# Kernel optimization log

Hardware: AMD Instinct MI355X
Metric: run time of the kernel (lower is better)

The kernel has to match this reference:

```python
import jax, jax.numpy as jnp
import numpy as np
import math

D_MODEL = 512; NHEAD = 8; D_HEAD = 64; C_OUT = 64
SEQ_LEN = 1024; PRED_LEN = 256; K = 8; DIM_FF = 2048
LOW_FREQ = 1; EPS = 1e-5
BATCH = 8


def _next_fast_len(n):
    # smallest 5-smooth integer >= n (matches scipy.fftpack.next_fast_len)
    while True:
        m = n
        for p in (2, 3, 5):
            while m % p == 0:
                m //= p
        if m == 1:
            return n
        n += 1


def _conv1d_fft(f, g, n):
    # matches torch conv1d_fft with N == M == n along axis 1 (cross-correlation via conj)
    fast_len = _next_fast_len(2 * n - 1)
    Ff = jnp.fft.rfft(f, n=fast_len, axis=1)
    Fg = jnp.fft.rfft(g, n=fast_len, axis=1)
    out = jnp.fft.irfft(Ff * jnp.conj(Fg), n=fast_len, axis=1)
    out = jnp.roll(out, -1, axis=1)
    return out[:, fast_len - n:fast_len]


def _exp_smooth(values, sw, v0, aux_values=None):
    # values: (b,t,h,d); sw: (h,1); v0: (1,1,h,d or 1)
    b, t, h, d = values.shape
    alpha = jax.nn.sigmoid(sw)                        # (h,1)
    powers = jnp.arange(t, dtype=values.dtype)
    weight = (1.0 - alpha) * alpha ** powers[::-1]    # (h,t)
    init_w = alpha ** (powers + 1.0)                  # (h,t)
    weight = weight.T[None, :, :, None]               # (1,t,h,1)
    init_w = init_w.T[None, :, :, None]
    out = init_w * v0 + _conv1d_fft(values, weight, t)
    if aux_values is not None:
        aux_w = weight * (alpha / (1.0 - alpha))[None, None, :, :]
        out = out + _conv1d_fft(aux_values, aux_w, t)
    return out


def _layer_norm(x, g, b):
    mu = x.mean(-1, keepdims=True)
    var = ((x - mu) ** 2).mean(-1, keepdims=True)
    return (x - mu) * jax.lax.rsqrt(var + EPS) * g + b


def _fourier_season(x):
    b, t, d = x.shape
    xf = jnp.fft.rfft(x, axis=1)                      # (b, t//2+1, d) complex
    hi = xf.shape[1] - 1 if t % 2 == 0 else xf.shape[1]
    xf = xf[:, LOW_FREQ:hi]                           # (b, F, d)
    freqs = (jnp.arange(t // 2 + 1, dtype=x.dtype) / t)[LOW_FREQ:hi]
    # top-K frequencies per (batch, feature) by amplitude
    _, idx = jax.lax.top_k(jnp.abs(jnp.moveaxis(xf, 1, 2)), K)   # (b,d,K)
    idx = jnp.moveaxis(idx, 2, 1)                     # (b,K,d)
    x_sel = jnp.take_along_axis(xf, idx, axis=1)      # (b,K,d) complex
    f_sel = freqs[idx]                                # (b,K,d)
    # trig re-synthesis / extrapolation over t + PRED_LEN steps
    x_all = jnp.concatenate([x_sel, jnp.conj(x_sel)], axis=1)    # (b,2K,d)
    f_all = jnp.concatenate([f_sel, -f_sel], axis=1)[:, :, None, :]  # (b,2K,1,d)
    t_val = jnp.arange(t + PRED_LEN, dtype=x.dtype).reshape(1, 1, -1, 1)
    amp = (jnp.abs(x_all) / t)[:, :, None, :]
    phase = jnp.angle(x_all)[:, :, None, :]
    x_time = amp * jnp.cos(2.0 * math.pi * f_all * t_val + phase)  # (b,2K,T,d)
    return x_time.sum(axis=1)                         # (b, t+PRED_LEN, d)


def _growth_layer(x, z0, in_w, in_b, sw, v0, out_w, out_b):
    b, t, _ = x.shape
    v = (x @ in_w.T + in_b).reshape(b, t, NHEAD, D_HEAD)
    v = jnp.concatenate([jnp.broadcast_to(z0[None, None], (b, 1, NHEAD, D_HEAD)), v], axis=1)
    v = v[:, 1:] - v[:, :-1]                          # first differences, (b,t,h,dh)
    s = _exp_smooth(v, sw, v0)
    s = jnp.concatenate([jnp.broadcast_to(v0, (b, 1, NHEAD, D_HEAD)), s], axis=1)  # (b,t+1,h,dh)
    return s.reshape(b, t + 1, NHEAD * D_HEAD) @ out_w.T + out_b


def _level_layer(level, growth, season, sw, v0, gw, gb, spw, spb):
    b, t, _ = level.shape
    g = (growth @ gw.T + gb)[..., None]               # (b,t,c,1)
    s = (season @ spw.T + spb)[..., None]             # (b,t,c,1)
    l = level[..., None] - s
    out = _exp_smooth(l, sw, v0, aux_values=g)        # (b,t,c,1)
    return out[..., 0]


def _forward(res, level, gl_z0, gl_in_w, gl_in_b, gl_sw, gl_v0, gl_out_w, gl_out_b,
             ll_sw, ll_v0, ll_gw, ll_gb, ll_sw2, ll_sb, ff_w1, ff_w2,
             n1_g, n1_b, n2_g, n2_b):
    season = _fourier_season(res)                     # (b, t+P, d)
    res = res - season[:, :-PRED_LEN]
    growth = _growth_layer(res, gl_z0, gl_in_w, gl_in_b, gl_sw, gl_v0, gl_out_w, gl_out_b)  # (b,t+1,d)
    res = _layer_norm(res - growth[:, 1:], n1_g, n1_b)
    ff = jax.nn.sigmoid(res @ ff_w1.T) @ ff_w2.T      # Feedforward, activation='sigmoid', no bias
    res = _layer_norm(res + ff, n2_g, n2_b)
    level = _level_layer(level, growth[:, :-1], season[:, :-PRED_LEN],
                         ll_sw, ll_v0, ll_gw, ll_gb, ll_sw2, ll_sb)
    return res, level, growth, season


def setup_inputs() -> dict:
    key = jax.random.key(0)
    ks = jax.random.split(key, 16)
    f32 = jnp.float32
    rn = lambda k, shape, s=1.0: jax.random.normal(k, shape, dtype=f32) * s
    return {
        "res": rn(ks[0], (BATCH, SEQ_LEN, D_MODEL)),
        "level": rn(ks[1], (BATCH, SEQ_LEN, C_OUT)),
        "gl_z0": rn(ks[2], (NHEAD, D_HEAD)),
        "gl_in_w": rn(ks[3], (NHEAD * D_HEAD, D_MODEL), 0.02),
        "gl_in_b": jnp.zeros((NHEAD * D_HEAD,), f32),
        "gl_sw": rn(ks[4], (NHEAD, 1)),
        "gl_v0": rn(ks[5], (1, 1, NHEAD, D_HEAD)),
        "gl_out_w": rn(ks[6], (D_MODEL, NHEAD * D_HEAD), 0.02),
        "gl_out_b": jnp.zeros((D_MODEL,), f32),
        "ll_sw": rn(ks[7], (C_OUT, 1)),
        "ll_v0": rn(ks[8], (1, 1, C_OUT, 1)),
        "ll_gw": rn(ks[9], (C_OUT, D_MODEL), 0.02),
        "ll_gb": jnp.zeros((C_OUT,), f32),
        "ll_sw2": rn(ks[10], (C_OUT, D_MODEL), 0.02),
        "ll_sb": jnp.zeros((C_OUT,), f32),
        "ff_w1": rn(ks[11], (DIM_FF, D_MODEL), 0.02),
        "ff_w2": rn(ks[12], (D_MODEL, DIM_FF), 0.02),
        "n1_g": jnp.ones((D_MODEL,), f32),
        "n1_b": jnp.zeros((D_MODEL,), f32),
        "n2_g": jnp.ones((D_MODEL,), f32),
        "n2_b": jnp.zeros((D_MODEL,), f32),
    }


def reference(res, level, gl_z0, gl_in_w, gl_in_b, gl_sw, gl_v0, gl_out_w, gl_out_b,
              ll_sw, ll_v0, ll_gw, ll_gb, ll_sw2, ll_sb, ff_w1, ff_w2,
              n1_g, n1_b, n2_g, n2_b):
    return _forward(res, level, gl_z0, gl_in_w, gl_in_b, gl_sw, gl_v0, gl_out_w, gl_out_b,
                    ll_sw, ll_v0, ll_gw, ll_gb, ll_sw2, ll_sb, ff_w1, ff_w2,
                    n1_g, n1_b, n2_g, n2_b)
```

## Files before the change

kernel.cpp:

```cpp
#include <hip/hip_runtime.h>
#include <hip/hip_bf16.h>
#include <math.h>

#define B_ 8
#define T_ 1024
#define D_ 512
#define PRED 256
#define TP (T_ + PRED)
#define NH 8
#define DH 64
#define DFF 2048
#define CO 64
#define KSEL 8

typedef __hip_bfloat16 bf16;
using bf16x8 = __attribute__((ext_vector_type(8))) short;
using f32x4  = __attribute__((ext_vector_type(4))) float;

__device__ __forceinline__ void gload_lds16(const void* gp, void* lp) {
  __builtin_amdgcn_global_load_lds(
      (const __attribute__((address_space(1))) void*)gp,
      (__attribute__((address_space(3))) void*)lp, 16, 0, 0);
}

template <int N>
__device__ __forceinline__ void vm_wait() {
  if constexpr (N == 0)      asm volatile("s_waitcnt vmcnt(0)" ::: "memory");
  else if constexpr (N == 2) asm volatile("s_waitcnt vmcnt(2)" ::: "memory");
  else if constexpr (N == 4) asm volatile("s_waitcnt vmcnt(4)" ::: "memory");
  else if constexpr (N == 6) asm volatile("s_waitcnt vmcnt(6)" ::: "memory");
  else if constexpr (N == 8) asm volatile("s_waitcnt vmcnt(8)" ::: "memory");
  else static_assert(N == 0, "unsupported vmcnt literal");
}

__global__ __launch_bounds__(256) void k_transpose(const float* __restrict__ in, float* __restrict__ out) {
  __shared__ float tile[32][33];
  const int b = blockIdx.z;
  const int d0 = blockIdx.x * 32, t0 = blockIdx.y * 32;
  const int tx = threadIdx.x, ty = threadIdx.y;
  const float* src = in + ((size_t)b * T_ + t0) * D_ + d0;
#pragma unroll
  for (int i = 0; i < 32; i += 8) tile[ty + i][tx] = src[(size_t)(ty + i) * D_ + tx];
  __syncthreads();
  float* dst = out + ((size_t)b * D_ + d0) * T_ + t0;
#pragma unroll
  for (int i = 0; i < 32; i += 8) dst[(size_t)(ty + i) * T_ + tx] = tile[tx][ty + i];
}

__global__ __launch_bounds__(256) void k_fft_topk(const float* __restrict__ xt, float* __restrict__ comp) {
  __shared__ float2 bA[512], bB[512], tw[256];
  __shared__ float xre[512], xim[512], mag2[512];
  __shared__ float wvv[4];
  __shared__ int wkk[4];
  __shared__ int selk[KSEL];
  const int j = threadIdx.x;
  const int bd = blockIdx.x;
  {
    float ang = -(6.283185307179586f / 512.0f) * (float)j;
    float sn, cs;
    sincosf(ang, &sn, &cs);
    tw[j] = make_float2(cs, sn);
  }
  const float4 v4 = ((const float4*)(xt + (size_t)bd * 1024))[j];
  bA[2 * j] = make_float2(v4.x, v4.y);
  bA[2 * j + 1] = make_float2(v4.z, v4.w);
  __syncthreads();
#pragma unroll
  for (int st = 0; st < 9; ++st) {
    const int s = 1 << st;
    const int p = j >> st;
    const int q = j & (s - 1);
    const int m = 256 >> st;
    float2 a, b2;
    if ((st & 1) == 0) { a = bA[q + s * p]; b2 = bA[q + s * (p + m)]; }
    else               { a = bB[q + s * p]; b2 = bB[q + s * (p + m)]; }
    const float2 w = tw[p << st];
    float2 d0 = make_float2(a.x + b2.x, a.y + b2.y);
    const float ex = a.x - b2.x, ey = a.y - b2.y;
    float2 d1 = make_float2(ex * w.x - ey * w.y, ex * w.y + ey * w.x);
    if ((st & 1) == 0) { bB[q + s * 2 * p] = d0; bB[q + s * (2 * p + 1)] = d1; }
    else               { bA[q + s * 2 * p] = d0; bA[q + s * (2 * p + 1)] = d1; }
    __syncthreads();
  }
#pragma unroll
  for (int u = 0; u < 2; ++u) {
    const int k = (u == 0) ? (j + 1) : (j + 257);
    if (k <= 511) {
      const float2 zk = bB[k & 511];
      const float2 zm = bB[(512 - k) & 511];
      const float Ex = 0.5f * (zk.x + zm.x), Ey = 0.5f * (zk.y - zm.y);
      const float Ox = 0.5f * (zk.y + zm.y), Oy = 0.5f * (zm.x - zk.x);
      float sn, cs;
      sincosf(-(6.283185307179586f / 1024.0f) * (float)k, &sn, &cs);
      const float Xr = Ex + cs * Ox - sn * Oy;
      const float Xi = Ey + cs * Oy + sn * Ox;
      xre[k] = Xr; xim[k] = Xi; mag2[k] = Xr * Xr + Xi * Xi;
    }
  }
  if (j == 0) mag2[0] = -1.0f;
  __syncthreads();
  const int lane = j & 63, wvi = j >> 6;
  for (int r = 0; r < KSEL; ++r) {
    float bv = mag2[j];
    int bk = j;
    const float v2 = mag2[j + 256];
    if (v2 > bv) { bv = v2; bk = j + 256; }
#pragma unroll
    for (int off = 32; off; off >>= 1) {
      const float ov = __shfl_down(bv, off);
      const int ok = __shfl_down(bk, off);
      if (ov > bv || (ov == bv && ok < bk)) { bv = ov; bk = ok; }
    }
    if (lane == 0) { wvv[wvi] = bv; wkk[wvi] = bk; }
    __syncthreads();
    if (j == 0) {
      float fv = wvv[0];
      int fk = wkk[0];
#pragma unroll
      for (int i = 1; i < 4; i++)
        if (wvv[i] > fv || (wvv[i] == fv && wkk[i] < fk)) { fv = wvv[i]; fk = wkk[i]; }
      selk[r] = fk;
      mag2[fk] = -2.0f;
    }
    __syncthreads();
  }
  if (j < KSEL) {
    const int k = selk[j];
    const float re = xre[k], im = xim[k];
    float* o = comp + (size_t)bd * 24 + j * 3;
    o[0] = 2.0f * sqrtf(re * re + im * im) * (1.0f / 1024.0f);
    o[1] = (float)k;
    o[2] = atan2f(im, re);
  }
}

__global__ __launch_bounds__(512) void k_season(const float* __restrict__ comp, const float* __restrict__ res,
                                                float* __restrict__ season, bf16* __restrict__ res1b,
                                                bf16* __restrict__ seasb) {
  const int d = threadIdx.x;
  const int b = blockIdx.y;
  const int t0 = blockIdx.x * 5;
  float a_[8], kf_[8], ph_[8];
  const float* c = comp + ((size_t)b * 512 + d) * 24;
#pragma unroll
  for (int i = 0; i < 8; i++) { a_[i] = c[3 * i]; kf_[i] = c[3 * i + 1]; ph_[i] = c[3 * i + 2]; }
#pragma unroll
  for (int tt = 0; tt < 5; ++tt) {
    const int t = t0 + tt;
    float acc = 0.0f;
#pragma unroll
    for (int i = 0; i < 8; i++) {
      float fr = kf_[i] * (float)t * (1.0f / 1024.0f);
      fr -= floorf(fr);
      acc += a_[i] * __cosf(fmaf(6.283185307179586f, fr, ph_[i]));
    }
    season[((size_t)b * TP + t) * D_ + d] = acc;
    if (t < T_) {
      const float rr = res[((size_t)b * T_ + t) * D_ + d] - acc;
      res1b[((size_t)b * T_ + t) * D_ + d] = __float2bfloat16(rr);
      seasb[((size_t)b * T_ + t) * D_ + d] = __float2bfloat16(acc);
    }
  }
}

#define CVT_TOTAL 2686976
__global__ __launch_bounds__(256) void k_cvt_all(const float* __restrict__ s0, const float* __restrict__ s1,
                                                 const float* __restrict__ s2_, const float* __restrict__ s3,
                                                 const float* __restrict__ s4, const float* __restrict__ s5,
                                                 bf16* __restrict__ dst) {
  const int i = (blockIdx.x * 256 + threadIdx.x) * 4;
  if (i >= CVT_TOTAL) return;
  const float* src;
  int off;
  if (i < 262144)       { src = s0;  off = i; }
  else if (i < 524288)  { src = s1;  off = i - 262144; }
  else if (i < 1572864) { src = s2_; off = i - 524288; }
  else if (i < 2621440) { src = s3;  off = i - 1572864; }
  else if (i < 2654208) { src = s4;  off = i - 2621440; }
  else                  { src = s5;  off = i - 2654208; }
  const float4 v = *(const float4*)(src + off);
  bf16* o = dst + i;
  o[0] = __float2bfloat16(v.x); o[1] = __float2bfloat16(v.y);
  o[2] = __float2bfloat16(v.z); o[3] = __float2bfloat16(v.w);
}

__global__ __launch_bounds__(1024) void k_growth_scan2(const float* __restrict__ v, const float* __restrict__ z0,
                                                       const float* __restrict__ sw, const float* __restrict__ v0,
                                                       bf16* __restrict__ s2) {
  const int b = blockIdx.x >> 3;
  const int col = (blockIdx.x & 7) * 64 + (threadIdx.x & 63);
  const int w = threadIdx.x >> 6;
  const float alpha = 1.0f / (1.0f + expf(-sw[col >> 6]));
  const float om = 1.0f - alpha;
  float a64 = alpha;
#pragma unroll
  for (int i = 0; i < 6; i++) a64 *= a64;
  const float* vp = v + (size_t)b * T_ * D_ + col;
  float vprev = (w == 0) ? z0[col] : vp[(size_t)(64 * w - 1) * D_];
  float sloc = 0.0f;
#pragma unroll 8
  for (int j = 0; j < 64; j++) {
    const float nv = vp[(size_t)(64 * w + j) * D_];
    sloc = alpha * sloc + om * (nv - vprev);
    vprev = nv;
  }
  __shared__ float lb[16][64], lc[16][64];
  lb[w][threadIdx.x & 63] = sloc;
  __syncthreads();
  if (w == 0) {
    float s = v0[col];
#pragma unroll
    for (int k = 0; k < 16; k++) { lc[k][threadIdx.x & 63] = s; s = a64 * s + lb[k][threadIdx.x & 63]; }
  }
  __syncthreads();
  float s = lc[w][threadIdx.x & 63];
  vprev = (w == 0) ? z0[col] : vp[(size_t)(64 * w - 1) * D_];
  bf16* op = s2 + (size_t)b * (T_ + 1) * D_ + col;
  if (w == 0) op[0] = __float2bfloat16(v0[col]);
#pragma unroll 8
  for (int j = 0; j < 64; j++) {
    const float nv = vp[(size_t)(64 * w + j) * D_];
    s = alpha * s + om * (nv - vprev);
    vprev = nv;
    op[(size_t)(64 * w + j + 1) * D_] = __float2bfloat16(s);
  }
}

__global__ __launch_bounds__(1024) void k_level_scan2(const float* __restrict__ level, const float* __restrict__ gp,
                                                      const float* __restrict__ sp, const float* __restrict__ sw,
                                                      const float* __restrict__ v0, float* __restrict__ out) {
  const int b = blockIdx.x;
  const int w = threadIdx.x >> 6;
  const int c = threadIdx.x & 63;
  const float alpha = 1.0f / (1.0f + expf(-sw[c]));
  const float om = 1.0f - alpha;
  float a64 = alpha;
#pragma unroll
  for (int i = 0; i < 6; i++) a64 *= a64;
  const size_t base = ((size_t)b * T_ + 64 * w) * CO + c;
  float sloc = 0.0f;
#pragma unroll 8
  for (int j = 0; j < 64; j++) {
    const size_t idx = base + (size_t)j * CO;
    const float u = om * (level[idx] - sp[idx]) + alpha * gp[idx];
    out[idx] = u;
    sloc = alpha * sloc + u;
  }
  __shared__ float lb[16][64], lc[16][64];
  lb[w][c] = sloc;
  __syncthreads();
  if (w == 0) {
    float s = v0[c];
#pragma unroll
    for (int k = 0; k < 16; k++) { lc[k][c] = s; s = a64 * s + lb[k][c]; }
  }
  __syncthreads();
  float s = lc[w][c];
#pragma unroll 8
  for (int j = 0; j < 64; j++) {
    const size_t idx = base + (size_t)j * CO;
    s = alpha * s + out[idx];
    out[idx] = s;
  }
}

template <int MODE>
__global__ __launch_bounds__(128) void k_ln(const float* __restrict__ x1, const float* __restrict__ x2,
                                            const float* __restrict__ x3, const float* __restrict__ g,
                                            const float* __restrict__ be, float* __restrict__ outF,
                                            bf16* __restrict__ outB) {
  const int m = blockIdx.x, tid = threadIdx.x;
  const int b = m >> 10;
  float4 v = ((const float4*)(x1 + (size_t)m * D_))[tid];
  if (MODE == 0) {
    const float4 se = ((const float4*)(x2 + ((size_t)(m + b * PRED)) * D_))[tid];
    const float4 gr = ((const float4*)(x3 + ((size_t)(m + b + 1)) * D_))[tid];
    v.x -= se.x + gr.x; v.y -= se.y + gr.y; v.z -= se.z + gr.z; v.w -= se.w + gr.w;
  }
  float s = v.x + v.y + v.z + v.w;
  float s2 = v.x * v.x + v.y * v.y + v.z * v.z + v.w * v.w;
#pragma unroll
  for (int off = 32; off; off >>= 1) { s += __shfl_down(s, off); s2 += __shfl_down(s2, off); }
  __shared__ float p1[2], p2[2];
  if ((tid & 63) == 0) { p1[tid >> 6] = s; p2[tid >> 6] = s2; }
  __syncthreads();
  const float S = p1[0] + p1[1], S2 = p2[0] + p2[1];
  const float mu = S * (1.0f / 512.0f);
  const float rs = rsqrtf(fmaxf(S2 * (1.0f / 512.0f) - mu * mu, 0.0f) + 1e-5f);
  const float4 gg = ((const float4*)g)[tid], bb = ((const float4*)be)[tid];
  float4 o;
  o.x = (v.x - mu) * rs * gg.x + bb.x;
  o.y = (v.y - mu) * rs * gg.y + bb.y;
  o.z = (v.z - mu) * rs * gg.z + bb.z;
  o.w = (v.w - mu) * rs * gg.w + bb.w;
  ((float4*)(outF + (size_t)m * D_))[tid] = o;
  if (MODE == 0) {
    bf16* ob = outB + (size_t)m * D_ + tid * 4;
    ob[0] = __float2bfloat16(o.x); ob[1] = __float2bfloat16(o.y);
    ob[2] = __float2bfloat16(o.z); ob[3] = __float2bfloat16(o.w);
  }
}

template <int BM, int BN, int BK, int EPI>
__global__ __launch_bounds__(256) void k_gemm(const bf16* __restrict__ A, const bf16* __restrict__ Bw,
                                              const float* __restrict__ bias, float* outF, bf16* __restrict__ outB,
                                              const float* resid, const int M, const int N, const int K,
                                              const int extra) {
  constexpr int WC = (BN >= 128) ? 2 : 1;
  constexpr int WR = 4 / WC;
  constexpr int FM = BM / (WR * 16);
  constexpr int FN = BN / (WC * 16);
  constexpr int RPC = 512 / BK;
  constexpr int LA = (BM / RPC) / 4, LB = (BN / RPC) / 4;
  constexpr int KK = BK / 32;
  constexpr int TLOADS = LA + LB;
  static_assert(LA >= 1 && LB >= 1, "tile too small for staging split");
  __shared__ bf16 lsA[2][BM * BK];
  __shared__ bf16 lsB[2][BN * BK];
  const int tid = threadIdx.x;
  const int w = tid >> 6, lane = tid & 63;
  const int tn = blockIdx.x, tm = blockIdx.y;
  const int wr = w / WC, wc = w % WC;
  const int r16 = lane & 15, hi = lane >> 4;

  int srowoff, scoloff;
  if constexpr (BK == 64) {
    const int rr = lane >> 3, cs = lane & 7;
    srowoff = rr;
    scoloff = (cs ^ rr) * 8;
  } else {
    const int sr = lane >> 3, cs = lane & 7;
    const int idx = cs ^ (sr & 7);
    srowoff = sr * 2 + (idx >> 2);
    scoloff = (idx & 3) * 8;
  }

  const f32x4 fzero = {0.f, 0.f, 0.f, 0.f};
  f32x4 acc[FM][FN];
#pragma unroll
  for (int i = 0; i < FM; i++)
#pragma unroll
    for (int jj = 0; jj < FN; jj++) acc[i][jj] = fzero;

  const int NT = K / BK;

  auto stage = [&](int kt, int sel) {
#pragma unroll
    for (int q = 0; q < LA; q++) {
      const int g = w * LA + q;
      int m = tm * BM + g * RPC + srowoff;
      if (m > M - 1) m = M - 1;
      m += (m >> 10) * extra;
      gload_lds16(A + (size_t)m * K + (size_t)kt * BK + scoloff, &lsA[sel][g * 512]);
    }
#pragma unroll
    for (int q = 0; q < LB; q++) {
      const int g = w * LB + q;
      const int n = tn * BN + g * RPC + srowoff;
      gload_lds16(Bw + (size_t)n * K + (size_t)kt * BK + scoloff, &lsB[sel][g * 512]);
    }
  };

  auto frag = [&](const bf16* ls, int row, int cc) -> bf16x8 {
    if constexpr (BK == 64) {
      const int g = row >> 3, rr = row & 7;
      return *(const bf16x8*)&ls[g * 512 + rr * 64 + ((cc ^ rr) << 3)];
    } else {
      const int g = row >> 4, rr = row & 15, sr = rr >> 1;
      const int idx = ((rr & 1) << 2) | cc;
      return *(const bf16x8*)&ls[g * 512 + sr * 64 + ((idx ^ (sr & 7)) << 3)];
    }
  };

  stage(0, 0);
  for (int kt = 0; kt < NT; ++kt) {
    const int sel = kt & 1;
    if (kt + 1 < NT) {
      stage(kt + 1, sel ^ 1);
      vm_wait<TLOADS>();
    } else {
      vm_wait<0>();
    }
    __builtin_amdgcn_sched_barrier(0);
    __builtin_amdgcn_s_barrier();
    __builtin_amdgcn_sched_barrier(0);
#pragma unroll
    for (int kk = 0; kk < KK; ++kk) {
      bf16x8 af[FM], bfv[FN];
#pragma unroll
      for (int i = 0; i < FM; i++)
        af[i] = frag(lsA[sel], wr * (FM * 16) + i * 16 + r16, kk * 4 + hi);
#pragma unroll
      for (int jj = 0; jj < FN; jj++)
        bfv[jj] = frag(lsB[sel], wc * (FN * 16) + jj * 16 + r16, kk * 4 + hi);
#pragma unroll
      for (int i = 0; i < FM; i++)
#pragma unroll
        for (int jj = 0; jj < FN; jj++)
          acc[i][jj] = __builtin_amdgcn_mfma_f32_16x16x32_bf16(af[i], bfv[jj], acc[i][jj], 0, 0, 0);
    }
    if (kt + 1 < NT) {
      __builtin_amdgcn_sched_barrier(0);
      __builtin_amdgcn_s_barrier();
      __builtin_amdgcn_sched_barrier(0);
    }
  }

#pragma unroll
  for (int i = 0; i < FM; i++) {
#pragma unroll
    for (int r = 0; r < 4; r++) {
      const int m = tm * BM + wr * (FM * 16) + i * 16 + hi * 4 + r;
      if (m < M) {
#pragma unroll
        for (int jj = 0; jj < FN; jj++) {
          const int n = tn * BN + wc * (FN * 16) + jj * 16 + r16;
          float x = acc[i][jj][r];
          if (bias) x += bias[n];
          const size_t idx = (size_t)m * N + n;
          if (EPI == 0) {
            outF[idx] = x;
          } else if (EPI == 1) {
            outF[idx] = x;
            outB[idx] = __float2bfloat16(x);
          } else if (EPI == 2) {
            outB[idx] = __float2bfloat16(1.0f / (1.0f + __expf(-x)));
          } else {
            outF[idx] = x + resid[idx];
          }
        }
      }
    }
  }
}

#define MB (size_t)(1u << 20)
static const size_t OFF_A = 0;
static const size_t OFF_C = 32 * MB;
static const size_t OFF_D = 40 * MB;
static const size_t OFF_E = 48 * MB;
static const size_t OFF_F = 54 * MB;
static const size_t OFF_G = 63 * MB;
static const size_t OFF_H = 72 * MB;
static const size_t OFF_J = 88 * MB;
static const size_t OFF_K = 89 * MB;
static const size_t OFF_K2 = 91 * MB;

#define W_IN 0
#define W_OUT 262144
#define W_FF1 524288
#define W_FF2 1572864
#define W_GW 2621440
#define W_SW2 2654208

extern "C" void kernel_launch(void* const* d_in, const int* in_sizes, int n_in, void* d_out, int out_size,
                              void* d_ws, size_t ws_size, hipStream_t stream) {
  (void)in_sizes; (void)n_in; (void)out_size; (void)ws_size;
  const float* res = (const float*)d_in[0];
  const float* level = (const float*)d_in[1];
  const float* gl_z0 = (const float*)d_in[2];
  const float* gl_in_w = (const float*)d_in[3];
  const float* gl_in_b = (const float*)d_in[4];
  const float* gl_sw = (const float*)d_in[5];
  const float* gl_v0 = (const float*)d_in[6];
  const float* gl_out_w = (const float*)d_in[7];
  const float* gl_out_b = (const float*)d_in[8];
  const float* ll_sw = (const float*)d_in[9];
  const float* ll_v0 = (const float*)d_in[10];
  const float* ll_gw = (const float*)d_in[11];
  const float* ll_gb = (const float*)d_in[12];
  const float* ll_sw2 = (const float*)d_in[13];
  const float* ll_sb = (const float*)d_in[14];
  const float* ff_w1 = (const float*)d_in[15];
  const float* ff_w2 = (const float*)d_in[16];
  const float* n1_g = (const float*)d_in[17];
  const float* n1_b = (const float*)d_in[18];
  const float* n2_g = (const float*)d_in[19];
  const float* n2_b = (const float*)d_in[20];

  char* ws = (char*)d_ws;
  float* resT = (float*)(ws + OFF_A);
  float* vbuf = (float*)(ws + OFF_A);
  bf16* hbuf = (bf16*)(ws + OFF_A);
  bf16* res1b = (bf16*)(ws + OFF_C);
  bf16* res2b = (bf16*)(ws + OFF_C);
  bf16* seasb = (bf16*)(ws + OFF_D);
  bf16* wE = (bf16*)(ws + OFF_E);
  bf16* s2b = (bf16*)(ws + OFF_F);
  bf16* grob = (bf16*)(ws + OFF_G);
  float* res2f = (float*)(ws + OFF_H);
  float* comp = (float*)(ws + OFF_J);
  float* gproj = (float*)(ws + OFF_K);
  float* sproj = (float*)(ws + OFF_K2);

  float* o_res = (float*)d_out;
  float* o_level = o_res + 4194304;
  float* o_growth = o_level + 524288;
  float* o_season = o_growth + 4198400;

  k_transpose<<<dim3(16, 32, 8), dim3(32, 8), 0, stream>>>(res, resT);
  k_fft_topk<<<4096, 256, 0, stream>>>(resT, comp);
  k_season<<<dim3(256, 8), 512, 0, stream>>>(comp, res, o_season, res1b, seasb);
  k_cvt_all<<<(CVT_TOTAL / 4 + 255) / 256, 256, 0, stream>>>(gl_in_w, gl_out_w, ff_w1, ff_w2, ll_gw, ll_sw2, wE);
  k_gemm<64, 128, 64, 0><<<dim3(4, 128), 256, 0, stream>>>(res1b, wE + W_IN, gl_in_b, vbuf, nullptr, nullptr, 8192, 512, 512, 0);
  k_growth_scan2<<<64, 1024, 0, stream>>>(vbuf, gl_z0, gl_sw, gl_v0, s2b);
  k_gemm<64, 128, 64, 1><<<dim3(4, 129), 256, 0, stream>>>(s2b, wE + W_OUT, gl_out_b, o_growth, grob, nullptr, 8200, 512, 512, 0);
  k_ln<0><<<8192, 128, 0, stream>>>(res, o_season, o_growth, n1_g, n1_b, res2f, res2b);
  k_gemm<128, 128, 32, 2><<<dim3(16, 64), 256, 0, stream>>>(res2b, wE + W_FF1, nullptr, nullptr, hbuf, nullptr, 8192, 2048, 512, 0);
  k_gemm<64, 128, 64, 3><<<dim3(4, 128), 256, 0, stream>>>(hbuf, wE + W_FF2, nullptr, res2f, nullptr, res2f, 8192, 512, 2048, 0);
  k_ln<1><<<8192, 128, 0, stream>>>(res2f, nullptr, nullptr, n2_g, n2_b, o_res, nullptr);
  k_gemm<64, 64, 64, 0><<<dim3(1, 128), 256, 0, stream>>>(grob, wE + W_GW, ll_gb, gproj, nullptr, nullptr, 8192, 64, 512, 1);
  k_gemm<64, 64, 64, 0><<<dim3(1, 128), 256, 0, stream>>>(seasb, wE + W_SW2, ll_sb, sproj, nullptr, nullptr, 8192, 64, 512, 0);
  k_level_scan2<<<8, 1024, 0, stream>>>(level, gproj, sproj, ll_sw, ll_v0, o_level);
}
```

Baseline: 243.8 us.

## Add dedicated FF1 GEMM kernel keeping full A row-panel resident in LDS

Measured after the change: 282.4 us. 15.8% more time.

```diff
diff --git a/kernel.cpp b/kernel.cpp
--- a/kernel.cpp
+++ b/kernel.cpp
@@ -298,6 +298,99 @@
     bf16* ob = outB + (size_t)m * D_ + tid * 4;
     ob[0] = __float2bfloat16(o.x); ob[1] = __float2bfloat16(o.y);
     ob[2] = __float2bfloat16(o.z); ob[3] = __float2bfloat16(o.w);
+  }
+}
+
+__global__ __launch_bounds__(256) void k_ff1(const bf16* __restrict__ A, const bf16* __restrict__ Bw,
+                                             bf16* __restrict__ outB) {
+  constexpr int Kc = 512, Nc = 2048, P = 128;
+  __shared__ bf16 lsA[64 * 512];
+  __shared__ bf16 lsB[3][128 * 32];
+  const int tid = threadIdx.x;
+  const int w = tid >> 6, lane = tid & 63;
+  const int ng = blockIdx.x, tm = blockIdx.y;
+  const int wr = w >> 1, wc = w & 1;
+  const int r16 = lane & 15, hi = lane >> 4;
+
+  const int sr = lane >> 3, cs = lane & 7;
+  const int bidx = cs ^ (sr & 7);
+  const int srowoff = sr * 2 + (bidx >> 2);
+  const int scoloff = (bidx & 3) * 8;
+
+  auto stageB = [&](int p, int sel) {
+    const int nt = p >> 4, kt = p & 15;
+#pragma unroll
+    for (int q = 0; q < 2; q++) {
+      const int g = w * 2 + q;
+      const int n = ng * 1024 + nt * 128 + g * 16 + srowoff;
+      gload_lds16(Bw + (size_t)n * Kc + kt * 32 + scoloff, &lsB[sel][g * 512]);
+    }
+  };
+
+#pragma unroll
+  for (int q = 0; q < 16; q++) {
+    const int r = w * 16 + q;
+    const int m = tm * 64 + r;
+    gload_lds16(A + (size_t)m * Kc + ((lane ^ (r & 7)) << 3), &lsA[r * 512]);
+  }
+  stageB(0, 0);
+  stageB(1, 1);
+  vm_wait<2>();
+  __builtin_amdgcn_sched_barrier(0);
+  __builtin_amdgcn_s_barrier();
+  __builtin_amdgcn_sched_barrier(0);
+
+  const f32x4 fz = {0.f, 0.f, 0.f, 0.f};
+  f32x4 acc[2][4];
+#pragma unroll
+  for (int i = 0; i < 2; i++)
+#pragma unroll
+    for (int jj = 0; jj < 4; jj++) acc[i][jj] = fz;
+
+  for (int p = 0; p < P; ++p) {
+    const int sel = p % 3;
+    const int kt = p & 15;
+    if (p + 2 < P) stageB(p + 2, (p + 2) % 3);
+    bf16x8 af[2], bfv[4];
+#pragma unroll
+    for (int i = 0; i < 2; i++) {
+      const int row = wr * 32 + i * 16 + r16;
+      const int cc = kt * 4 + hi;
+      af[i] = *(const bf16x8*)&lsA[row * 512 + ((cc ^ (row & 7)) << 3)];
+    }
+#pragma unroll
+    for (int jj = 0; jj < 4; jj++) {
+      const int row = wc * 64 + jj * 16 + r16;
+      const int g = row >> 4, rr = row & 15, sr2 = rr >> 1;
+      const int idx = ((rr & 1) << 2) | hi;
+      bfv[jj] = *(const bf16x8*)&lsB[sel][g * 512 + sr2 * 64 + ((idx ^ (sr2 & 7)) << 3)];
+    }
+#pragma unroll
+    for (int i = 0; i < 2; i++)
+#pragma unroll
+      for (int jj = 0; jj < 4; jj++)
+        acc[i][jj] = __builtin_amdgcn_mfma_f32_16x16x32_bf16(af[i], bfv[jj], acc[i][jj], 0, 0, 0);
+    if (kt == 15) {
+      const int nt = p >> 4;
+#pragma unroll
+      for (int i = 0; i < 2; i++)
+#pragma unroll
+        for (int r = 0; r < 4; r++) {
+          const int m = tm * 64 + wr * 32 + i * 16 + hi * 4 + r;
+#pragma unroll
+          for (int jj = 0; jj < 4; jj++) {
+            const int n = ng * 1024 + nt * 128 + wc * 64 + jj * 16 + r16;
+            outB[(size_t)m * Nc + n] = __float2bfloat16(1.0f / (1.0f + __expf(-acc[i][jj][r])));
+            acc[i][jj][r] = 0.0f;
+          }
+        }
+    }
+    if (p + 1 < P) {
+      if (p + 2 < P) vm_wait<2>(); else vm_wait<0>();
+      __builtin_amdgcn_sched_barrier(0);
+      __builtin_amdgcn_s_barrier();
+      __builtin_amdgcn_sched_barrier(0);
+    }
   }
 }
 
@@ -506,7 +599,7 @@
   k_growth_scan2<<<64, 1024, 0, stream>>>(vbuf, gl_z0, gl_sw, gl_v0, s2b);
   k_gemm<64, 128, 64, 1><<<dim3(4, 129), 256, 0, stream>>>(s2b, wE + W_OUT, gl_out_b, o_growth, grob, nullptr, 8200, 512, 512, 0);
   k_ln<0><<<8192, 128, 0, stream>>>(res, o_season, o_growth, n1_g, n1_b, res2f, res2b);
-  k_gemm<128, 128, 32, 2><<<dim3(16, 64), 256, 0, stream>>>(res2b, wE + W_FF1, nullptr, nullptr, hbuf, nullptr, 8192, 2048, 512, 0);
+  k_ff1<<<dim3(2, 128), 256, 0, stream>>>(res2b, wE + W_FF1, hbuf);
   k_gemm<64, 128, 64, 3><<<dim3(4, 128), 256, 0, stream>>>(hbuf, wE + W_FF2, nullptr, res2f, nullptr, res2f, 8192, 512, 2048, 0);
   k_ln<1><<<8192, 128, 0, stream>>>(res2f, nullptr, nullptr, n2_g, n2_b, o_res, nullptr);
   k_gemm<64, 64, 64, 0><<<dim3(1, 128), 256, 0, stream>>>(grob, wE + W_GW, ll_gb, gproj, nullptr, nullptr, 8192, 64, 512, 1);
```
